# Optimization experiments

Measured on AMD Instinct MI355X. Metric: run time of the kernel, lower is better.

## Reference

```python
import jax, jax.numpy as jnp
import numpy as np

N_NODES = 100000
N_EDGES = 1600000
NEG_SLOPE = 0.2
EPS = 1e-16


def gat_conv(x, edge_index, W, att_src, att_dst, bias, heads, out_ch, concat):
    # x: [N, F_in]; edge_index: [2, E] with edge (src j -> dst i)
    N = x.shape[0]
    src, dst = edge_index[0], edge_index[1]
    h = (x @ W).reshape(N, heads, out_ch)              # [N, H, C]
    a_src = (h * att_src[None]).sum(-1)                # [N, H]
    a_dst = (h * att_dst[None]).sum(-1)                # [N, H]
    e = a_src[src] + a_dst[dst]                        # [E, H]
    e = jnp.where(e > 0, e, NEG_SLOPE * e)             # LeakyReLU(0.2)
    # segment softmax over destination node
    m = jax.ops.segment_max(e, dst, num_segments=N)    # [N, H]
    m = jnp.where(jnp.isfinite(m), m, 0.0)
    ex = jnp.exp(e - m[dst])                           # [E, H]
    s = jax.ops.segment_sum(ex, dst, num_segments=N)   # [N, H]
    alpha = ex / (s[dst] + EPS)                        # [E, H]
    msg = h[src] * alpha[..., None]                    # [E, H, C]
    out = jax.ops.segment_sum(msg, dst, num_segments=N)  # [N, H, C]
    if concat:
        out = out.reshape(N, heads * out_ch)
    else:
        out = out.mean(axis=1)
    return out + bias


def setup_inputs() -> dict:
    key = jax.random.key(0)
    ks = jax.random.split(key, 8)
    x = jax.random.normal(ks[0], (N_NODES, 2), dtype=jnp.float32)
    edge_index = jax.random.randint(ks[1], (2, N_EDGES), 0, N_NODES, dtype=jnp.int64)
    glorot = lambda k, shape, fan: jax.random.normal(k, shape, jnp.float32) * (1.0 / np.sqrt(fan))
    W1 = glorot(ks[2], (2, 128), 2)
    att_src1 = glorot(ks[3], (8, 16), 16)
    att_dst1 = glorot(ks[4], (8, 16), 16)
    b1 = jnp.zeros((128,), jnp.float32)
    W2 = glorot(ks[5], (128, 4), 128)
    att_src2 = glorot(ks[6], (1, 4), 4)
    att_dst2 = glorot(ks[7], (1, 4), 4)
    b2 = jnp.zeros((4,), jnp.float32)
    return {"x": x, "edge_index": edge_index, "W1": W1, "att_src1": att_src1,
            "att_dst1": att_dst1, "b1": b1, "W2": W2, "att_src2": att_src2,
            "att_dst2": att_dst2, "b2": b2}


def reference(x, edge_index, W1, att_src1, att_dst1, b1, W2, att_src2, att_dst2, b2):
    h = gat_conv(x, edge_index, W1, att_src1, att_dst1, b1, heads=8, out_ch=16, concat=True)
    h = jax.nn.relu(h)
    # dropout p=0.6 is identity in eval mode
    h = gat_conv(h, edge_index, W2, att_src2, att_dst2, b2, heads=1, out_ch=4, concat=True)
    return jax.nn.log_softmax(h, axis=1)
```

## Files before the change

kernel.cpp:

```cpp
#include <hip/hip_runtime.h>
#include <math.h>

static constexpr float kNegSlope = 0.2f;
static constexpr float kEps = 1e-16f;
static constexpr int SLICES = 256;
static constexpr int BSHIFT = 7;
static constexpr int BMASK = 127;
static constexpr unsigned SRCMASK = 0x1FFFFu;
static constexpr int CAP = 2816;

__device__ __forceinline__ float leaky(float v) {
    return v > 0.0f ? v : kNegSlope * v;
}


__global__ __launch_bounds__(512) void k_hist1(const int* __restrict__ ei,
                                               int* __restrict__ table,
                                               int* __restrict__ rowptr,
                                               int E, int N, int NBUCK) {
    __shared__ int hist[832];
    int b = blockIdx.x, t = threadIdx.x;
    if (b == 0 && t == 0) rowptr[N] = E;
    for (int i = t; i < NBUCK; i += 512) hist[i] = 0;
    __syncthreads();
    int S = (((E + SLICES - 1) / SLICES) + 3) & ~3;
    int lo = b * S, hi = min(lo + S, E);
    for (int i = lo + t * 4; i < hi; i += 512 * 4) {
        int4 dv = *(const int4*)(ei + E + i);
        atomicAdd(&hist[dv.x >> BSHIFT], 1);
        atomicAdd(&hist[dv.y >> BSHIFT], 1);
        atomicAdd(&hist[dv.z >> BSHIFT], 1);
        atomicAdd(&hist[dv.w >> BSHIFT], 1);
    }
    __syncthreads();
    for (int i = t; i < NBUCK; i += 512) table[i * SLICES + b] = hist[i];
}

__global__ __launch_bounds__(256) void k_scan_reduce(const int* __restrict__ src,
                                                     int* __restrict__ partial, int n) {
    __shared__ int wsum[4];
    int b = blockIdx.x, t = threadIdx.x;
    int base = b * 1024 + t * 4;
    int s = 0;
#pragma unroll
    for (int k = 0; k < 4; ++k) {
        int idx = base + k;
        s += (idx < n) ? src[idx] : 0;
    }
#pragma unroll
    for (int off = 1; off < 64; off <<= 1) s += __shfl_xor(s, off);
    if ((t & 63) == 0) wsum[t >> 6] = s;
    __syncthreads();
    if (t == 0) partial[b] = wsum[0] + wsum[1] + wsum[2] + wsum[3];
}

__global__ __launch_bounds__(256) void k_scan_apply(int* __restrict__ data,
                                                    const int* __restrict__ partial,
                                                    int n, int nsb) {
    __shared__ int sm[8];
    __shared__ int baseSh;
    int b = blockIdx.x, t = threadIdx.x;
    int acc = 0;
    for (int i = t; i < b; i += 256) acc += partial[i];
#pragma unroll
    for (int off = 1; off < 64; off <<= 1) acc += __shfl_xor(acc, off);
    if ((t & 63) == 0) sm[t >> 6] = acc;
    __syncthreads();
    if (t == 0) baseSh = sm[0] + sm[1] + sm[2] + sm[3];
    __syncthreads();
    int chunkBase = baseSh;
    __syncthreads();
    int base = b * 1024 + t * 4;
    int v[4];
#pragma unroll
    for (int k = 0; k < 4; ++k) {
        int idx = base + k;
        v[k] = (idx < n) ? data[idx] : 0;
    }
    int sum4 = v[0] + v[1] + v[2] + v[3];
    int s = sum4;
#pragma unroll
    for (int off = 1; off < 64; off <<= 1) {
        int u = __shfl_up(s, off);
        if ((t & 63) >= off) s += u;
    }
    if ((t & 63) == 63) sm[t >> 6] = s;
    __syncthreads();
    int woff = 0;
    int w = t >> 6;
    for (int ww = 0; ww < w; ++ww) woff += sm[ww];
    int ex = chunkBase + woff + (s - sum4);
#pragma unroll
    for (int k = 0; k < 4; ++k) {
        int idx = base + k;
        if (idx < n) data[idx] = ex;
        ex += v[k];
    }
}

__global__ __launch_bounds__(512) void k_bin2(const int* __restrict__ ei,
                                              const int* __restrict__ table,
                                              unsigned* __restrict__ sbuf, int E, int NBUCK) {
    __shared__ int cur[832];
    int b = blockIdx.x, t = threadIdx.x;
    for (int i = t; i < NBUCK; i += 512) cur[i] = table[i * SLICES + b];
    __syncthreads();
    int S = (((E + SLICES - 1) / SLICES) + 3) & ~3;
    int lo = b * S, hi = min(lo + S, E);
    for (int i = lo + t * 4; i < hi; i += 512 * 4) {
        int4 sv = *(const int4*)(ei + i);
        int4 dv = *(const int4*)(ei + E + i);
        int pos;
        pos = atomicAdd(&cur[dv.x >> BSHIFT], 1);
        sbuf[pos] = (unsigned)sv.x | ((unsigned)(dv.x & BMASK) << 17);
        pos = atomicAdd(&cur[dv.y >> BSHIFT], 1);
        sbuf[pos] = (unsigned)sv.y | ((unsigned)(dv.y & BMASK) << 17);
        pos = atomicAdd(&cur[dv.z >> BSHIFT], 1);
        sbuf[pos] = (unsigned)sv.z | ((unsigned)(dv.z & BMASK) << 17);
        pos = atomicAdd(&cur[dv.w >> BSHIFT], 1);
        sbuf[pos] = (unsigned)sv.w | ((unsigned)(dv.w & BMASK) << 17);
    }
}

__global__ __launch_bounds__(512, 4) void k_bfinal_g1(
        const unsigned* __restrict__ sbuf, const int* __restrict__ table,
        int* __restrict__ rowptr, int* __restrict__ ssrc,
        const float* __restrict__ x,
        const float* __restrict__ W1, const float* __restrict__ att_src1,
        const float* __restrict__ att_dst1, const float* __restrict__ b1,
        const float* __restrict__ W2, float* __restrict__ h2,
        int N, int E, int NBUCK) {
    __shared__ int hist[128];
    __shared__ int sc[128];
    __shared__ int excl[128];
    __shared__ int cur[128];
    __shared__ unsigned raws[CAP];
    __shared__ int sls[CAP];
    __shared__ float pbuf[32];
    int b = blockIdx.x;
    int t = threadIdx.x;
    int lo = table[b * SLICES];
    int hi = (b + 1 < NBUCK) ? table[(b + 1) * SLICES] : E;
    int cnt = hi - lo;
    bool inLds = (cnt <= CAP);

    if (t < 128) hist[t] = 0;
    if (t >= 128 && t < 160) {
        int u = t - 128;
        int which = u >> 4;
        int hd = u & 15;
        int h = hd >> 1, d = hd & 1;
        const float* att = which ? att_dst1 : att_src1;
        float s = 0.0f;
#pragma unroll
        for (int c = 0; c < 16; ++c) s += W1[d * 128 + h * 16 + c] * att[h * 16 + c];
        pbuf[which * 16 + d * 8 + h] = s;
    }
    __syncthreads();

    if (inLds) {
        for (int i = t; i < cnt; i += 512) {
            unsigned v = sbuf[lo + i];
            raws[i] = v;
            atomicAdd(&hist[v >> 17], 1);
        }
    } else {
        for (int i = lo + t; i < hi; i += 512) atomicAdd(&hist[sbuf[i] >> 17], 1);
    }
    __syncthreads();

    if (t < 128) {
        int lane = t & 63;
        int own = hist[t];
        int v = own;
#pragma unroll
        for (int off = 1; off < 64; off <<= 1) {
            int u = __shfl_up(v, off);
            if (lane >= off) v += u;
        }
        sc[t] = v;
    }
    __syncthreads();
    if (t < 128) {
        int ex = sc[t] - hist[t] + (t >= 64 ? sc[63] : 0);
        excl[t] = ex;
        cur[t] = ex;
        int node = (b << BSHIFT) + t;
        if (node < N) rowptr[node] = lo + ex;
    }
    __syncthreads();

    if (inLds) {
        for (int i = t; i < cnt; i += 512) {
            unsigned v = raws[i];
            int pos = atomicAdd(&cur[v >> 17], 1);
            sls[pos] = (int)(v & SRCMASK);
        }
        __syncthreads();
        for (int i = t; i < cnt; i += 512) ssrc[lo + i] = sls[i];
    } else {
        for (int i = lo + t; i < hi; i += 512) {
            unsigned v = sbuf[i];
            int pos = atomicAdd(&cur[v >> 17], 1);
            ssrc[lo + pos] = (int)(v & SRCMASK);
        }
        __syncthreads();
    }
    __syncthreads();

    int dl = t >> 2, q = t & 3;
    int node = (b << BSHIFT) + dl;
    int st = excl[dl];
    int ecnt = hist[dl];
    float2 xn = ((const float2*)x)[min(node, N - 1)];
    float Ps0[8], Ps1[8], adv[8], l[8], s0[8], s1[8];
#pragma unroll
    for (int h = 0; h < 8; ++h) {
        Ps0[h] = pbuf[h];
        Ps1[h] = pbuf[8 + h];
        adv[h] = xn.x * pbuf[16 + h] + xn.y * pbuf[24 + h];
        l[h] = 0.f; s0[h] = 0.f; s1[h] = 0.f;
    }
    if (inLds) {
        for (int j = q; j < ecnt; j += 4) {
            int src = sls[st + j];
            float2 xs = ((const float2*)x)[src];
#pragma unroll
            for (int h = 0; h < 8; ++h) {
                float p = __expf(leaky(xs.x * Ps0[h] + xs.y * Ps1[h] + adv[h]));
                l[h] += p; s0[h] += p * xs.x; s1[h] += p * xs.y;
            }
        }
    } else {
        for (int j = q; j < ecnt; j += 4) {
            int src = ssrc[lo + st + j];
            float2 xs = ((const float2*)x)[src];
#pragma unroll
            for (int h = 0; h < 8; ++h) {
                float p = __expf(leaky(xs.x * Ps0[h] + xs.y * Ps1[h] + adv[h]));
                l[h] += p; s0[h] += p * xs.x; s1[h] += p * xs.y;
            }
        }
    }
#pragma unroll
    for (int off = 1; off < 4; off <<= 1) {
#pragma unroll
        for (int h = 0; h < 8; ++h) {
            l[h] += __shfl_xor(l[h], off);
            s0[h] += __shfl_xor(s0[h], off);
            s1[h] += __shfl_xor(s1[h], off);
        }
    }
    float h0 = 0.f, h1v = 0.f, h2v = 0.f, h3 = 0.f;
#pragma unroll
    for (int k = 0; k < 2; ++k) {
        int h = q + 4 * k;
        float inv = 1.0f / (l[h] + kEps);
        float sX0 = s0[h] * inv, sX1 = s1[h] * inv;
#pragma unroll
        for (int c = 0; c < 16; ++c) {
            int col = h * 16 + c;
            float o = fmaxf(W1[col] * sX0 + W1[128 + col] * sX1 + b1[col], 0.0f);
            h0 += o * W2[col * 4 + 0];
            h1v += o * W2[col * 4 + 1];
            h2v += o * W2[col * 4 + 2];
            h3 += o * W2[col * 4 + 3];
        }
    }
#pragma unroll
    for (int off = 1; off < 4; off <<= 1) {
        h0 += __shfl_xor(h0, off);
        h1v += __shfl_xor(h1v, off);
        h2v += __shfl_xor(h2v, off);
        h3 += __shfl_xor(h3, off);
    }
    if (node < N && q == 0) {
        ((float4*)h2)[node] = make_float4(h0, h1v, h2v, h3);
    }
}

__global__ __launch_bounds__(256) void k_gather2_out(
        const int* __restrict__ rowptr, const int* __restrict__ ssrc,
        const float* __restrict__ h2, const float* __restrict__ att_src2,
        const float* __restrict__ att_dst2, const float* __restrict__ b2,
        float* __restrict__ out, int N) {
    int idx = blockIdx.x * blockDim.x + threadIdx.x;
    int n = idx >> 3, q = idx & 7;
    if (n >= N) return;
    int start = rowptr[n], end = rowptr[n + 1];
    float4 as2 = *(const float4*)att_src2;
    float4 ad2v = *(const float4*)att_dst2;
    float4 hn = ((const float4*)h2)[n];
    float ad = hn.x * ad2v.x + hn.y * ad2v.y + hn.z * ad2v.z + hn.w * ad2v.w;
    float l = 0.0f;
    float4 acc = make_float4(0.f, 0.f, 0.f, 0.f);
    for (int j = start + q; j < end; j += 8) {
        int src = ssrc[j];
        float4 hv = ((const float4*)h2)[src];
        float e = hv.x * as2.x + hv.y * as2.y + hv.z * as2.z + hv.w * as2.w + ad;
        float p = __expf(leaky(e));
        l += p;
        acc.x += p * hv.x; acc.y += p * hv.y; acc.z += p * hv.z; acc.w += p * hv.w;
    }
#pragma unroll
    for (int off = 1; off < 8; off <<= 1) {
        l += __shfl_xor(l, off);
        acc.x += __shfl_xor(acc.x, off);
        acc.y += __shfl_xor(acc.y, off);
        acc.z += __shfl_xor(acc.z, off);
        acc.w += __shfl_xor(acc.w, off);
    }
    if (q == 0) {
        float inv = 1.0f / (l + kEps);
        float4 v = make_float4(acc.x * inv + b2[0], acc.y * inv + b2[1],
                               acc.z * inv + b2[2], acc.w * inv + b2[3]);
        float mx = fmaxf(fmaxf(v.x, v.y), fmaxf(v.z, v.w));
        float sum = __expf(v.x - mx) + __expf(v.y - mx) + __expf(v.z - mx) + __expf(v.w - mx);
        float lse = mx + logf(sum);
        ((float4*)out)[n] = make_float4(v.x - lse, v.y - lse, v.z - lse, v.w - lse);
    }
}

extern "C" void kernel_launch(void* const* d_in, const int* in_sizes, int n_in,
                              void* d_out, int out_size, void* d_ws, size_t ws_size,
                              hipStream_t stream) {
    const float* x        = (const float*)d_in[0];
    const int*   ei       = (const int*)d_in[1];
    const float* W1       = (const float*)d_in[2];
    const float* att_src1 = (const float*)d_in[3];
    const float* att_dst1 = (const float*)d_in[4];
    const float* b1       = (const float*)d_in[5];
    const float* W2       = (const float*)d_in[6];
    const float* att_src2 = (const float*)d_in[7];
    const float* att_dst2 = (const float*)d_in[8];
    const float* b2       = (const float*)d_in[9];

    const int N = in_sizes[0] / 2;
    const int E = in_sizes[1] / 2;
    const int NBUCK = (N + BMASK) >> BSHIFT;
    const int ntable = NBUCK * SLICES;
    const int nsb = (ntable + 1023) / 1024;

    int* table     = (int*)d_ws;
    int* partial   = table + ntable + 64;
    int* rowptr    = partial + 1024;
    int* ssrc      = rowptr + ((N + 4) & ~3);
    unsigned* sbuf = (unsigned*)(ssrc + E);
    float* h2      = (float*)(sbuf + E);

    k_hist1<<<SLICES, 512, 0, stream>>>(ei, table, rowptr, E, N, NBUCK);
    k_scan_reduce<<<nsb, 256, 0, stream>>>(table, partial, ntable);
    k_scan_apply<<<nsb, 256, 0, stream>>>(table, partial, ntable, nsb);
    k_bin2<<<SLICES, 512, 0, stream>>>(ei, table, sbuf, E, NBUCK);

    k_bfinal_g1<<<NBUCK, 512, 0, stream>>>(sbuf, table, rowptr, ssrc, x,
                                           W1, att_src1, att_dst1, b1, W2, h2,
                                           N, E, NBUCK);

    k_gather2_out<<<(N * 8 + 255) / 256, 256, 0, stream>>>(rowptr, ssrc, h2,
                                                           att_src2, att_dst2, b2,
                                                           (float*)d_out, N);
}
```

Measured before the change: 168.6 us.

## Split fused bucket-sort and layer-1 gather into separate kernels

The fused kernel that sorted edges within each destination bucket and then ran the layer-1 attention gather is split into a sort-only kernel and a standalone gather kernel. The gather now uses 8 lanes per node reading CSR from global memory, instead of 4 lanes per node reading sorted sources from LDS. The aim is higher occupancy and parallelism for the gather, which is no longer tied to the sort kernel's large LDS footprint and launch bounds. In exchange it adds a kernel launch and an extra global round trip of the sorted source array.

```diff
diff --git a/kernel.cpp b/kernel.cpp
--- a/kernel.cpp
+++ b/kernel.cpp
@@ -122,21 +122,15 @@
     }
 }
 
-__global__ __launch_bounds__(512, 4) void k_bfinal_g1(
+__global__ __launch_bounds__(512) void k_sort(
         const unsigned* __restrict__ sbuf, const int* __restrict__ table,
         int* __restrict__ rowptr, int* __restrict__ ssrc,
-        const float* __restrict__ x,
-        const float* __restrict__ W1, const float* __restrict__ att_src1,
-        const float* __restrict__ att_dst1, const float* __restrict__ b1,
-        const float* __restrict__ W2, float* __restrict__ h2,
         int N, int E, int NBUCK) {
     __shared__ int hist[128];
     __shared__ int sc[128];
-    __shared__ int excl[128];
     __shared__ int cur[128];
     __shared__ unsigned raws[CAP];
     __shared__ int sls[CAP];
-    __shared__ float pbuf[32];
     int b = blockIdx.x;
     int t = threadIdx.x;
     int lo = table[b * SLICES];
@@ -145,17 +139,6 @@
     bool inLds = (cnt <= CAP);
 
     if (t < 128) hist[t] = 0;
-    if (t >= 128 && t < 160) {
-        int u = t - 128;
-        int which = u >> 4;
-        int hd = u & 15;
-        int h = hd >> 1, d = hd & 1;
-        const float* att = which ? att_dst1 : att_src1;
-        float s = 0.0f;
-#pragma unroll
-        for (int c = 0; c < 16; ++c) s += W1[d * 128 + h * 16 + c] * att[h * 16 + c];
-        pbuf[which * 16 + d * 8 + h] = s;
-    }
     __syncthreads();
 
     if (inLds) {
@@ -183,7 +166,6 @@
     __syncthreads();
     if (t < 128) {
         int ex = sc[t] - hist[t] + (t >= 64 ? sc[63] : 0);
-        excl[t] = ex;
         cur[t] = ex;
         int node = (b << BSHIFT) + t;
         if (node < N) rowptr[node] = lo + ex;
@@ -204,15 +186,35 @@
             int pos = atomicAdd(&cur[v >> 17], 1);
             ssrc[lo + pos] = (int)(v & SRCMASK);
         }
-        __syncthreads();
-    }
-    __syncthreads();
-
-    int dl = t >> 2, q = t & 3;
-    int node = (b << BSHIFT) + dl;
-    int st = excl[dl];
-    int ecnt = hist[dl];
-    float2 xn = ((const float2*)x)[min(node, N - 1)];
+    }
+}
+
+__global__ __launch_bounds__(256) void k_gather1(
+        const int* __restrict__ rowptr, const int* __restrict__ ssrc,
+        const float* __restrict__ x,
+        const float* __restrict__ W1, const float* __restrict__ att_src1,
+        const float* __restrict__ att_dst1, const float* __restrict__ b1,
+        const float* __restrict__ W2, float* __restrict__ h2, int N) {
+    __shared__ float pbuf[32];
+    int t = threadIdx.x;
+    if (t < 32) {
+        int which = t >> 4;
+        int hd = t & 15;
+        int h = hd >> 1, d = hd & 1;
+        const float* att = which ? att_dst1 : att_src1;
+        float s = 0.0f;
+#pragma unroll
+        for (int c = 0; c < 16; ++c) s += W1[d * 128 + h * 16 + c] * att[h * 16 + c];
+        pbuf[which * 16 + d * 8 + h] = s;
+    }
+    __syncthreads();
+
+    int idx = blockIdx.x * blockDim.x + t;
+    int n = idx >> 3, q = idx & 7;
+    if (n >= N) return;
+    const float2* x2 = (const float2*)x;
+    int start = rowptr[n], end = rowptr[n + 1];
+    float2 xn = x2[n];
     float Ps0[8], Ps1[8], adv[8], l[8], s0[8], s1[8];
 #pragma unroll
     for (int h = 0; h < 8; ++h) {
@@ -221,29 +223,17 @@
         adv[h] = xn.x * pbuf[16 + h] + xn.y * pbuf[24 + h];
         l[h] = 0.f; s0[h] = 0.f; s1[h] = 0.f;
     }
-    if (inLds) {
-        for (int j = q; j < ecnt; j += 4) {
-            int src = sls[st + j];
-            float2 xs = ((const float2*)x)[src];
-#pragma unroll
-            for (int h = 0; h < 8; ++h) {
-                float p = __expf(leaky(xs.x * Ps0[h] + xs.y * Ps1[h] + adv[h]));
-                l[h] += p; s0[h] += p * xs.x; s1[h] += p * xs.y;
-            }
-        }
-    } else {
-        for (int j = q; j < ecnt; j += 4) {
-            int src = ssrc[lo + st + j];
-            float2 xs = ((const float2*)x)[src];
-#pragma unroll
-            for (int h = 0; h < 8; ++h) {
-                float p = __expf(leaky(xs.x * Ps0[h] + xs.y * Ps1[h] + adv[h]));
-                l[h] += p; s0[h] += p * xs.x; s1[h] += p * xs.y;
-            }
-        }
-    }
-#pragma unroll
-    for (int off = 1; off < 4; off <<= 1) {
+    for (int j = start + q; j < end; j += 8) {
+        int src = ssrc[j];
+        float2 xs = x2[src];
+#pragma unroll
+        for (int h = 0; h < 8; ++h) {
+            float p = __expf(leaky(xs.x * Ps0[h] + xs.y * Ps1[h] + adv[h]));
+            l[h] += p; s0[h] += p * xs.x; s1[h] += p * xs.y;
+        }
+    }
+#pragma unroll
+    for (int off = 1; off < 8; off <<= 1) {
 #pragma unroll
         for (int h = 0; h < 8; ++h) {
             l[h] += __shfl_xor(l[h], off);
@@ -252,14 +242,12 @@
         }
     }
     float h0 = 0.f, h1v = 0.f, h2v = 0.f, h3 = 0.f;
-#pragma unroll
-    for (int k = 0; k < 2; ++k) {
-        int h = q + 4 * k;
-        float inv = 1.0f / (l[h] + kEps);
-        float sX0 = s0[h] * inv, sX1 = s1[h] * inv;
+    {
+        float inv = 1.0f / (l[q] + kEps);
+        float sX0 = s0[q] * inv, sX1 = s1[q] * inv;
 #pragma unroll
         for (int c = 0; c < 16; ++c) {
-            int col = h * 16 + c;
+            int col = q * 16 + c;
             float o = fmaxf(W1[col] * sX0 + W1[128 + col] * sX1 + b1[col], 0.0f);
             h0 += o * W2[col * 4 + 0];
             h1v += o * W2[col * 4 + 1];
@@ -268,14 +256,14 @@
         }
     }
 #pragma unroll
-    for (int off = 1; off < 4; off <<= 1) {
+    for (int off = 1; off < 8; off <<= 1) {
         h0 += __shfl_xor(h0, off);
         h1v += __shfl_xor(h1v, off);
         h2v += __shfl_xor(h2v, off);
         h3 += __shfl_xor(h3, off);
     }
-    if (node < N && q == 0) {
-        ((float4*)h2)[node] = make_float4(h0, h1v, h2v, h3);
+    if (q == 0) {
+        ((float4*)h2)[n] = make_float4(h0, h1v, h2v, h3);
     }
 }
 
@@ -353,9 +341,11 @@
     k_scan_apply<<<nsb, 256, 0, stream>>>(table, partial, ntable, nsb);
     k_bin2<<<SLICES, 512, 0, stream>>>(ei, table, sbuf, E, NBUCK);
 
-    k_bfinal_g1<<<NBUCK, 512, 0, stream>>>(sbuf, table, rowptr, ssrc, x,
-                                           W1, att_src1, att_dst1, b1, W2, h2,
-                                           N, E, NBUCK);
+    k_sort<<<NBUCK, 512, 0, stream>>>(sbuf, table, rowptr, ssrc, N, E, NBUCK);
+
+    k_gather1<<<(N * 8 + 255) / 256, 256, 0, stream>>>(rowptr, ssrc, x,
+                                                       W1, att_src1, att_dst1, b1,
+                                                       W2, h2, N);
 
     k_gather2_out<<<(N * 8 + 255) / 256, 256, 0, stream>>>(rowptr, ssrc, h2,
                                                            att_src2, att_dst2, b2,
```

Result: no change. 167.0 us (-1.0%).
